# Performance work log

Hardware: AMD Instinct MI355X
Metric: run time of the kernel (lower is better)

The kernel has to match this reference:

```python
import jax, jax.numpy as jnp
import numpy as np

EPS = 1e-6

def _feature_map(x):
    # elu(x) + 1 == where(x>0, x+1, exp(x))
    return jax.nn.elu(x) + 1.0

def setup_inputs() -> dict:
    key = jax.random.key(0)
    kq, kk, kv, km = jax.random.split(key, 4)
    B, H, S, D = 4, 16, 4096, 64
    query = jax.random.normal(kq, (B, H, S, D), dtype=jnp.float32)
    key_t = jax.random.normal(kk, (B, H, S, D), dtype=jnp.float32)
    value = jax.random.normal(kv, (B, H, S, D), dtype=jnp.float32)
    # True = padded position
    key_padding_mask = jax.random.bernoulli(km, 0.25, (B, S))
    return {"query": query, "key": key_t, "value": value,
            "key_padding_mask": key_padding_mask}

def reference(query, key, value, key_padding_mask):
    q = _feature_map(query)              # [B,H,S,D]
    k = _feature_map(key)
    v = value
    # valid = ~mask, broadcast over heads and feature dim
    valid = (~key_padding_mask)[:, None, :, None].astype(query.dtype)  # [B,1,S,1]
    k = k * valid
    v = v * valid
    kv = jnp.einsum('bhsd,bhsf->bhdf', k, v)              # [B,H,D,D]
    z = jnp.einsum('bhtd,bhd->bht', q, k.sum(axis=2)) + EPS
    out = jnp.einsum('bhtd,bhdf->bhtf', q, kv) / z[..., None]
    return out
```

## Files before the change

### kernel.cpp

```cpp
#include <hip/hip_runtime.h>

#define S_LEN 4096
#define D_DIM 64
#define NBH   64
#define EPS_F 1e-6f
#define PSZ   (D_DIM * D_DIM + D_DIM)

__device__ __forceinline__ float phi_f(float x) {
    return x > 0.0f ? x + 1.0f : __expf(x);
}

__global__ void detect_mask(const unsigned int* __restrict__ w,
                            unsigned int* __restrict__ flag) {
    __shared__ int all01, allf;
    if (threadIdx.x == 0) { all01 = 1; allf = 1; }
    __syncthreads();
    int a = 1, f = 1;
    for (int i = threadIdx.x; i < 4096; i += blockDim.x) {
        unsigned int v = w[i];
        if (v > 1u) a = 0;
        if (v != 0u && v != 0x3F800000u) f = 0;
    }
    if (!a) atomicExch(&all01, 0);
    if (!f) atomicExch(&allf, 0);
    __syncthreads();
    if (threadIdx.x == 0) *flag = all01 ? 0u : (allf ? 2u : 1u);
}

__global__ __launch_bounds__(256) void la_phase1(
    const float* __restrict__ K, const float* __restrict__ V,
    const void* __restrict__ mask, const unsigned int* __restrict__ flagp,
    float* __restrict__ partials, int CH)
{
    __shared__ float smem[2][4096];
    __shared__ float ksred[4][64];

    const int bh   = blockIdx.x;
    const int b    = bh >> 4;
    const unsigned int flag = *flagp;
    const int tid  = threadIdx.x;
    const int wave = tid >> 6;
    const int lane = tid & 63;
    const int tt   = lane >> 3;
    const int tf   = lane & 7;
    const int chunk = S_LEN / CH;
    const int NT    = chunk / 32;
    const int s0    = blockIdx.y * chunk;

    const float* Kbh = K + (size_t)bh * S_LEN * D_DIM;
    const float* Vbh = V + (size_t)bh * S_LEN * D_DIM;
    const int*           mi = (const int*)mask;
    const unsigned char* mb = (const unsigned char*)mask;
    const float*         mf = (const float*)mask;

    float acc[8][8];
    float ks[8];
    #pragma unroll
    for (int i = 0; i < 8; ++i) {
        ks[i] = 0.0f;
        #pragma unroll
        for (int j = 0; j < 8; ++j) acc[i][j] = 0.0f;
    }

    const int row0 = tid >> 4;
    const int col0 = (tid & 15) * 4;

    float4 kr[2], vr[2];
    int    pr[2];

    auto issue = [&](int ts) {
        #pragma unroll
        for (int p = 0; p < 2; ++p) {
            int row = p * 16 + row0;
            int s   = s0 + ts + row;
            int ml  = b * S_LEN + s;
            bool pad;
            if (flag == 0u)      pad = (mi[ml] != 0);
            else if (flag == 1u) pad = (mb[ml] != 0);
            else                 pad = (mf[ml] != 0.0f);
            pr[p] = pad ? 1 : 0;
            kr[p] = *reinterpret_cast<const float4*>(&Kbh[(size_t)s * D_DIM + col0]);
            vr[p] = *reinterpret_cast<const float4*>(&Vbh[(size_t)s * D_DIM + col0]);
        }
    };

    auto xstore = [&](int bufi) {
        #pragma unroll
        for (int p = 0; p < 2; ++p) {
            int row = p * 16 + row0;
            float4 k4 = kr[p], v4 = vr[p];
            if (pr[p]) {
                k4 = make_float4(0.f, 0.f, 0.f, 0.f);
                v4 = make_float4(0.f, 0.f, 0.f, 0.f);
            } else {
                k4.x = phi_f(k4.x); k4.y = phi_f(k4.y);
                k4.z = phi_f(k4.z); k4.w = phi_f(k4.w);
            }
            *reinterpret_cast<float4*>(&smem[bufi][row * 64 + col0])        = k4;
            *reinterpret_cast<float4*>(&smem[bufi][2048 + row * 64 + col0]) = v4;
        }
    };

    issue(0);
    xstore(0);
    __syncthreads();
    int cur = 0;
    for (int it = 0; it < NT; ++it) {
        if (it + 1 < NT) issue((it + 1) * 32);
        #pragma unroll
        for (int r = 0; r < 8; ++r) {
            const int row = wave * 8 + r;
            float kk[8], vv[8];
            *reinterpret_cast<float4*>(&kk[0]) = *reinterpret_cast<const float4*>(&smem[cur][row * 64 + tt * 8]);
            *reinterpret_cast<float4*>(&kk[4]) = *reinterpret_cast<const float4*>(&smem[cur][row * 64 + tt * 8 + 4]);
            *reinterpret_cast<float4*>(&vv[0]) = *reinterpret_cast<const float4*>(&smem[cur][2048 + row * 64 + tf * 8]);
            *reinterpret_cast<float4*>(&vv[4]) = *reinterpret_cast<const float4*>(&smem[cur][2048 + row * 64 + tf * 8 + 4]);
            #pragma unroll
            for (int i = 0; i < 8; ++i) {
                #pragma unroll
                for (int j = 0; j < 8; ++j)
                    acc[i][j] = fmaf(kk[i], vv[j], acc[i][j]);
                ks[i] += kk[i];
            }
        }
        if (it + 1 < NT) xstore(cur ^ 1);
        __syncthreads();
        cur ^= 1;
    }

    if (tf == 0) {
        #pragma unroll
        for (int i = 0; i < 8; ++i) ksred[wave][tt * 8 + i] = ks[i];
    }
    for (int w = 0; w < 4; ++w) {
        if (wave == w) {
            #pragma unroll
            for (int i = 0; i < 8; ++i) {
                float4* p0 = reinterpret_cast<float4*>(&smem[0][(tt * 8 + i) * 64 + tf * 8]);
                float4 a0 = make_float4(acc[i][0], acc[i][1], acc[i][2], acc[i][3]);
                float4 a1 = make_float4(acc[i][4], acc[i][5], acc[i][6], acc[i][7]);
                if (w == 0) { p0[0] = a0; p0[1] = a1; }
                else {
                    float4 c0 = p0[0], c1 = p0[1];
                    c0.x += a0.x; c0.y += a0.y; c0.z += a0.z; c0.w += a0.w;
                    c1.x += a1.x; c1.y += a1.y; c1.z += a1.z; c1.w += a1.w;
                    p0[0] = c0; p0[1] = c1;
                }
            }
        }
        __syncthreads();
    }

    float* pp = partials + ((size_t)(bh * CH + blockIdx.y)) * PSZ;
    #pragma unroll
    for (int q = 0; q < 4; ++q) {
        int fi = q * 256 + tid;
        reinterpret_cast<float4*>(pp)[fi] = reinterpret_cast<const float4*>(&smem[0][0])[fi];
    }
    if (tid < 64)
        pp[4096 + tid] = ksred[0][tid] + ksred[1][tid] + ksred[2][tid] + ksred[3][tid];
}

template <int CHT>
__global__ __launch_bounds__(256) void la_reduce_t(
    const float* __restrict__ partials, float* __restrict__ kv,
    float* __restrict__ ksum)
{
    const int bh = blockIdx.x;
    const int half = blockIdx.y;
    const float4* base = reinterpret_cast<const float4*>(partials + (size_t)bh * CHT * PSZ);
    const int hi = (half + 1) * 520;
    for (int idx = half * 520 + threadIdx.x; idx < hi; idx += 256) {
        float4 s = make_float4(0.f, 0.f, 0.f, 0.f);
        #pragma unroll
        for (int c = 0; c < CHT; ++c) {
            float4 v = base[(size_t)c * (PSZ / 4) + idx];
            s.x += v.x; s.y += v.y; s.z += v.z; s.w += v.w;
        }
        if (idx < 1024)
            reinterpret_cast<float4*>(kv + (size_t)bh * 4096)[idx] = s;
        else
            reinterpret_cast<float4*>(ksum + bh * 64)[idx - 1024] = s;
    }
}

__global__ __launch_bounds__(256) void la_phase2(
    const float* __restrict__ Q,
    const float* __restrict__ kv_ws, const float* __restrict__ ksum_ws,
    float* __restrict__ out)
{
    __shared__ float kvs[64][64];
    __shared__ float kss[64];

    const int bh   = blockIdx.x;
    const int tid  = threadIdx.x;
    const int wave = tid >> 6;
    const int lane = tid & 63;
    const int tt   = lane >> 3;
    const int tf   = lane & 7;
    const int t0   = blockIdx.y * 128 + wave * 32;

    const float* Qbh = Q + (size_t)bh * S_LEN * D_DIM;
    const float* kvb = kv_ws + (size_t)bh * D_DIM * D_DIM;

    #pragma unroll
    for (int p = 0; p < 4; ++p) {
        int fi = p * 256 + tid;
        reinterpret_cast<float4*>(kvs)[fi] = reinterpret_cast<const float4*>(kvb)[fi];
    }
    if (tid < 16)
        reinterpret_cast<float4*>(kss)[tid] =
            reinterpret_cast<const float4*>(ksum_ws + bh * D_DIM)[tid];
    __syncthreads();

    const float* qr0 = Qbh + (size_t)(t0 + tt) * D_DIM;

    float acc[4][8];
    float z[4];
    #pragma unroll
    for (int r = 0; r < 4; ++r) {
        z[r] = 0.0f;
        #pragma unroll
        for (int c = 0; c < 8; ++c) acc[r][c] = 0.0f;
    }

    float4 qn[4];
    #pragma unroll
    for (int r = 0; r < 4; ++r)
        qn[r] = *reinterpret_cast<const float4*>(qr0 + r * 8 * D_DIM);

    #pragma unroll 4
    for (int dq = 0; dq < 64; dq += 4) {
        float qc[4][4];
        #pragma unroll
        for (int r = 0; r < 4; ++r) {
            qc[r][0] = phi_f(qn[r].x); qc[r][1] = phi_f(qn[r].y);
            qc[r][2] = phi_f(qn[r].z); qc[r][3] = phi_f(qn[r].w);
        }
        const int dnext = (dq + 4) & 63;
        #pragma unroll
        for (int r = 0; r < 4; ++r)
            qn[r] = *reinterpret_cast<const float4*>(qr0 + r * 8 * D_DIM + dnext);
        float ks4[4];
        *reinterpret_cast<float4*>(ks4) = *reinterpret_cast<const float4*>(&kss[dq]);
        #pragma unroll
        for (int j = 0; j < 4; ++j) {
            float kvr[8];
            *reinterpret_cast<float4*>(&kvr[0]) = *reinterpret_cast<const float4*>(&kvs[dq + j][tf * 8]);
            *reinterpret_cast<float4*>(&kvr[4]) = *reinterpret_cast<const float4*>(&kvs[dq + j][tf * 8 + 4]);
            #pragma unroll
            for (int r = 0; r < 4; ++r) {
                z[r] = fmaf(qc[r][j], ks4[j], z[r]);
                #pragma unroll
                for (int c = 0; c < 8; ++c)
                    acc[r][c] = fmaf(qc[r][j], kvr[c], acc[r][c]);
            }
        }
    }

    #pragma unroll
    for (int r = 0; r < 4; ++r) {
        int t = t0 + tt + 8 * r;
        float inv = 1.0f / (z[r] + EPS_F);
        float o[8];
        #pragma unroll
        for (int c = 0; c < 8; ++c) o[c] = acc[r][c] * inv;
        float* op = out + ((size_t)bh * S_LEN + t) * D_DIM + tf * 8;
        *reinterpret_cast<float4*>(&op[0]) = *reinterpret_cast<const float4*>(&o[0]);
        *reinterpret_cast<float4*>(&op[4]) = *reinterpret_cast<const float4*>(&o[4]);
    }
}

extern "C" void kernel_launch(void* const* d_in, const int* in_sizes, int n_in,
                              void* d_out, int out_size, void* d_ws, size_t ws_size,
                              hipStream_t stream)
{
    (void)in_sizes; (void)n_in; (void)out_size;
    const float* Q   = (const float*)d_in[0];
    const float* K   = (const float*)d_in[1];
    const float* V   = (const float*)d_in[2];
    const void* mask = d_in[3];

    int CH = 16;
    while (CH > 1) {
        size_t need = ((size_t)NBH * CH * PSZ + (size_t)NBH * 4096 + NBH * 64) * 4 + 16;
        if (need <= ws_size) break;
        CH >>= 1;
    }
    float* partials = (float*)d_ws;
    float* kvf  = partials + (size_t)NBH * CH * PSZ;
    float* ksf  = kvf + (size_t)NBH * 4096;
    unsigned int* flag = (unsigned int*)(ksf + NBH * 64);

    detect_mask<<<1, 256, 0, stream>>>((const unsigned int*)mask, flag);
    la_phase1<<<dim3(NBH, CH), 256, 0, stream>>>(K, V, mask, flag, partials, CH);
    switch (CH) {
        case 16: la_reduce_t<16><<<dim3(NBH, 2), 256, 0, stream>>>(partials, kvf, ksf); break;
        case 8:  la_reduce_t<8> <<<dim3(NBH, 2), 256, 0, stream>>>(partials, kvf, ksf); break;
        case 4:  la_reduce_t<4> <<<dim3(NBH, 2), 256, 0, stream>>>(partials, kvf, ksf); break;
        case 2:  la_reduce_t<2> <<<dim3(NBH, 2), 256, 0, stream>>>(partials, kvf, ksf); break;
        default: la_reduce_t<1> <<<dim3(NBH, 2), 256, 0, stream>>>(partials, kvf, ksf); break;
    }
    la_phase2<<<dim3(NBH, 32), 256, 0, stream>>>(Q, kvf, ksf, (float*)d_out);
}
```

Measured before the change: 281.7 us.

## Read K/V and kv state directly from global memory, dropping LDS staging

```diff
diff --git a/kernel.cpp b/kernel.cpp
--- a/kernel.cpp
+++ b/kernel.cpp
@@ -32,7 +32,7 @@
     const void* __restrict__ mask, const unsigned int* __restrict__ flagp,
     float* __restrict__ partials, int CH)
 {
-    __shared__ float smem[2][4096];
+    __shared__ float red[4096];
     __shared__ float ksred[4][64];
 
     const int bh   = blockIdx.x;
@@ -44,14 +44,15 @@
     const int tt   = lane >> 3;
     const int tf   = lane & 7;
     const int chunk = S_LEN / CH;
-    const int NT    = chunk / 32;
-    const int s0    = blockIdx.y * chunk;
-
-    const float* Kbh = K + (size_t)bh * S_LEN * D_DIM;
-    const float* Vbh = V + (size_t)bh * S_LEN * D_DIM;
+    const int rpw   = chunk >> 2;
+    const int s0    = blockIdx.y * chunk + wave * rpw;
+
+    const float* Kr = K + ((size_t)bh * S_LEN + s0) * D_DIM;
+    const float* Vr = V + ((size_t)bh * S_LEN + s0) * D_DIM;
     const int*           mi = (const int*)mask;
     const unsigned char* mb = (const unsigned char*)mask;
     const float*         mf = (const float*)mask;
+    const int ml0 = b * S_LEN + s0;
 
     float acc[8][8];
     float ks[8];
@@ -62,59 +63,27 @@
         for (int j = 0; j < 8; ++j) acc[i][j] = 0.0f;
     }
 
-    const int row0 = tid >> 4;
-    const int col0 = (tid & 15) * 4;
-
-    float4 kr[2], vr[2];
-    int    pr[2];
-
-    auto issue = [&](int ts) {
-        #pragma unroll
-        for (int p = 0; p < 2; ++p) {
-            int row = p * 16 + row0;
-            int s   = s0 + ts + row;
-            int ml  = b * S_LEN + s;
-            bool pad;
-            if (flag == 0u)      pad = (mi[ml] != 0);
-            else if (flag == 1u) pad = (mb[ml] != 0);
-            else                 pad = (mf[ml] != 0.0f);
-            pr[p] = pad ? 1 : 0;
-            kr[p] = *reinterpret_cast<const float4*>(&Kbh[(size_t)s * D_DIM + col0]);
-            vr[p] = *reinterpret_cast<const float4*>(&Vbh[(size_t)s * D_DIM + col0]);
-        }
-    };
-
-    auto xstore = [&](int bufi) {
-        #pragma unroll
-        for (int p = 0; p < 2; ++p) {
-            int row = p * 16 + row0;
-            float4 k4 = kr[p], v4 = vr[p];
-            if (pr[p]) {
-                k4 = make_float4(0.f, 0.f, 0.f, 0.f);
-                v4 = make_float4(0.f, 0.f, 0.f, 0.f);
-            } else {
-                k4.x = phi_f(k4.x); k4.y = phi_f(k4.y);
-                k4.z = phi_f(k4.z); k4.w = phi_f(k4.w);
-            }
-            *reinterpret_cast<float4*>(&smem[bufi][row * 64 + col0])        = k4;
-            *reinterpret_cast<float4*>(&smem[bufi][2048 + row * 64 + col0]) = v4;
-        }
-    };
-
-    issue(0);
-    xstore(0);
-    __syncthreads();
-    int cur = 0;
-    for (int it = 0; it < NT; ++it) {
-        if (it + 1 < NT) issue((it + 1) * 32);
-        #pragma unroll
-        for (int r = 0; r < 8; ++r) {
-            const int row = wave * 8 + r;
+    for (int seg = 0; seg < rpw; seg += 64) {
+        int mvi;
+        {
+            const int ml = ml0 + seg + lane;
+            if (flag == 0u)      mvi = (mi[ml] != 0);
+            else if (flag == 1u) mvi = (mb[ml] != 0);
+            else                 mvi = (mf[ml] != 0.0f);
+        }
+        const float* Ks = Kr + (size_t)seg * D_DIM;
+        const float* Vs = Vr + (size_t)seg * D_DIM;
+        #pragma unroll 2
+        for (int r = 0; r < 64; ++r) {
+            const int pad = __shfl(mvi, r);
             float kk[8], vv[8];
-            *reinterpret_cast<float4*>(&kk[0]) = *reinterpret_cast<const float4*>(&smem[cur][row * 64 + tt * 8]);
-            *reinterpret_cast<float4*>(&kk[4]) = *reinterpret_cast<const float4*>(&smem[cur][row * 64 + tt * 8 + 4]);
-            *reinterpret_cast<float4*>(&vv[0]) = *reinterpret_cast<const float4*>(&smem[cur][2048 + row * 64 + tf * 8]);
-            *reinterpret_cast<float4*>(&vv[4]) = *reinterpret_cast<const float4*>(&smem[cur][2048 + row * 64 + tf * 8 + 4]);
+            *reinterpret_cast<float4*>(&kk[0]) = *reinterpret_cast<const float4*>(Ks + r * 64 + tt * 8);
+            *reinterpret_cast<float4*>(&kk[4]) = *reinterpret_cast<const float4*>(Ks + r * 64 + tt * 8 + 4);
+            *reinterpret_cast<float4*>(&vv[0]) = *reinterpret_cast<const float4*>(Vs + r * 64 + tf * 8);
+            *reinterpret_cast<float4*>(&vv[4]) = *reinterpret_cast<const float4*>(Vs + r * 64 + tf * 8 + 4);
+            #pragma unroll
+            for (int i = 0; i < 8; ++i)
+                kk[i] = pad ? 0.0f : phi_f(kk[i]);
             #pragma unroll
             for (int i = 0; i < 8; ++i) {
                 #pragma unroll
@@ -123,20 +92,18 @@
                 ks[i] += kk[i];
             }
         }
-        if (it + 1 < NT) xstore(cur ^ 1);
-        __syncthreads();
-        cur ^= 1;
     }
 
     if (tf == 0) {
         #pragma unroll
         for (int i = 0; i < 8; ++i) ksred[wave][tt * 8 + i] = ks[i];
     }
+    __syncthreads();
     for (int w = 0; w < 4; ++w) {
         if (wave == w) {
             #pragma unroll
             for (int i = 0; i < 8; ++i) {
-                float4* p0 = reinterpret_cast<float4*>(&smem[0][(tt * 8 + i) * 64 + tf * 8]);
+                float4* p0 = reinterpret_cast<float4*>(&red[(tt * 8 + i) * 64 + tf * 8]);
                 float4 a0 = make_float4(acc[i][0], acc[i][1], acc[i][2], acc[i][3]);
                 float4 a1 = make_float4(acc[i][4], acc[i][5], acc[i][6], acc[i][7]);
                 if (w == 0) { p0[0] = a0; p0[1] = a1; }
@@ -155,7 +122,7 @@
     #pragma unroll
     for (int q = 0; q < 4; ++q) {
         int fi = q * 256 + tid;
-        reinterpret_cast<float4*>(pp)[fi] = reinterpret_cast<const float4*>(&smem[0][0])[fi];
+        reinterpret_cast<float4*>(pp)[fi] = reinterpret_cast<const float4*>(red)[fi];
     }
     if (tid < 64)
         pp[4096 + tid] = ksred[0][tid] + ksred[1][tid] + ksred[2][tid] + ksred[3][tid];
@@ -189,9 +156,6 @@
     const float* __restrict__ kv_ws, const float* __restrict__ ksum_ws,
     float* __restrict__ out)
 {
-    __shared__ float kvs[64][64];
-    __shared__ float kss[64];
-
     const int bh   = blockIdx.x;
     const int tid  = threadIdx.x;
     const int wave = tid >> 6;
@@ -200,20 +164,9 @@
     const int tf   = lane & 7;
     const int t0   = blockIdx.y * 128 + wave * 32;
 
-    const float* Qbh = Q + (size_t)bh * S_LEN * D_DIM;
+    const float* qr0 = Q + ((size_t)bh * S_LEN + t0 + tt) * D_DIM;
     const float* kvb = kv_ws + (size_t)bh * D_DIM * D_DIM;
-
-    #pragma unroll
-    for (int p = 0; p < 4; ++p) {
-        int fi = p * 256 + tid;
-        reinterpret_cast<float4*>(kvs)[fi] = reinterpret_cast<const float4*>(kvb)[fi];
-    }
-    if (tid < 16)
-        reinterpret_cast<float4*>(kss)[tid] =
-            reinterpret_cast<const float4*>(ksum_ws + bh * D_DIM)[tid];
-    __syncthreads();
-
-    const float* qr0 = Qbh + (size_t)(t0 + tt) * D_DIM;
+    const float* ksb = ksum_ws + bh * D_DIM;
 
     float acc[4][8];
     float z[4];
@@ -224,30 +177,22 @@
         for (int c = 0; c < 8; ++c) acc[r][c] = 0.0f;
     }
 
-    float4 qn[4];
-    #pragma unroll
-    for (int r = 0; r < 4; ++r)
-        qn[r] = *reinterpret_cast<const float4*>(qr0 + r * 8 * D_DIM);
-
-    #pragma unroll 4
+    #pragma unroll 2
     for (int dq = 0; dq < 64; dq += 4) {
+        float ks4[4];
+        *reinterpret_cast<float4*>(ks4) = *reinterpret_cast<const float4*>(ksb + dq);
         float qc[4][4];
         #pragma unroll
         for (int r = 0; r < 4; ++r) {
-            qc[r][0] = phi_f(qn[r].x); qc[r][1] = phi_f(qn[r].y);
-            qc[r][2] = phi_f(qn[r].z); qc[r][3] = phi_f(qn[r].w);
-        }
-        const int dnext = (dq + 4) & 63;
-        #pragma unroll
-        for (int r = 0; r < 4; ++r)
-            qn[r] = *reinterpret_cast<const float4*>(qr0 + r * 8 * D_DIM + dnext);
-        float ks4[4];
-        *reinterpret_cast<float4*>(ks4) = *reinterpret_cast<const float4*>(&kss[dq]);
+            float4 q4 = *reinterpret_cast<const float4*>(qr0 + r * 8 * D_DIM + dq);
+            qc[r][0] = phi_f(q4.x); qc[r][1] = phi_f(q4.y);
+            qc[r][2] = phi_f(q4.z); qc[r][3] = phi_f(q4.w);
+        }
         #pragma unroll
         for (int j = 0; j < 4; ++j) {
             float kvr[8];
-            *reinterpret_cast<float4*>(&kvr[0]) = *reinterpret_cast<const float4*>(&kvs[dq + j][tf * 8]);
-            *reinterpret_cast<float4*>(&kvr[4]) = *reinterpret_cast<const float4*>(&kvs[dq + j][tf * 8 + 4]);
+            *reinterpret_cast<float4*>(&kvr[0]) = *reinterpret_cast<const float4*>(kvb + (dq + j) * 64 + tf * 8);
+            *reinterpret_cast<float4*>(&kvr[4]) = *reinterpret_cast<const float4*>(kvb + (dq + j) * 64 + tf * 8 + 4);
             #pragma unroll
             for (int r = 0; r < 4; ++r) {
                 z[r] = fmaf(qc[r][j], ks4[j], z[r]);
```

Result: slower. 352.6 us (+25.2%).

## Double phase1 threads, split D across waves, stage mask in LDS

Applied to the files above, without the earlier changes.

```diff
diff --git a/kernel.cpp b/kernel.cpp
--- a/kernel.cpp
+++ b/kernel.cpp
@@ -27,22 +27,25 @@
     if (threadIdx.x == 0) *flag = all01 ? 0u : (allf ? 2u : 1u);
 }
 
-__global__ __launch_bounds__(256) void la_phase1(
+__global__ __launch_bounds__(512) void la_phase1(
     const float* __restrict__ K, const float* __restrict__ V,
     const void* __restrict__ mask, const unsigned int* __restrict__ flagp,
     float* __restrict__ partials, int CH)
 {
     __shared__ float smem[2][4096];
+    __shared__ float mlds[2][32];
     __shared__ float ksred[4][64];
 
     const int bh   = blockIdx.x;
     const int b    = bh >> 4;
     const unsigned int flag = *flagp;
     const int tid  = threadIdx.x;
-    const int wave = tid >> 6;
+    const int wv   = tid >> 6;
     const int lane = tid & 63;
-    const int tt   = lane >> 3;
-    const int tf   = lane & 7;
+    const int rq   = wv >> 1;
+    const int dh   = wv & 1;
+    const int dgrp = lane >> 3;
+    const int fgrp = lane & 7;
     const int chunk = S_LEN / CH;
     const int NT    = chunk / 32;
     const int s0    = blockIdx.y * chunk;
@@ -53,52 +56,42 @@
     const unsigned char* mb = (const unsigned char*)mask;
     const float*         mf = (const float*)mask;
 
-    float acc[8][8];
-    float ks[8];
-    #pragma unroll
-    for (int i = 0; i < 8; ++i) {
+    float acc[4][8];
+    float ks[4];
+    #pragma unroll
+    for (int i = 0; i < 4; ++i) {
         ks[i] = 0.0f;
         #pragma unroll
         for (int j = 0; j < 8; ++j) acc[i][j] = 0.0f;
     }
 
-    const int row0 = tid >> 4;
-    const int col0 = (tid & 15) * 4;
-
-    float4 kr[2], vr[2];
-    int    pr[2];
+    const int srow = tid >> 4;
+    const int scol = (tid & 15) * 4;
+
+    float4 kr, vr;
+    float  mreg = 1.0f;
 
     auto issue = [&](int ts) {
-        #pragma unroll
-        for (int p = 0; p < 2; ++p) {
-            int row = p * 16 + row0;
-            int s   = s0 + ts + row;
-            int ml  = b * S_LEN + s;
+        const int s = s0 + ts + srow;
+        kr = *reinterpret_cast<const float4*>(&Kbh[(size_t)s * D_DIM + scol]);
+        vr = *reinterpret_cast<const float4*>(&Vbh[(size_t)s * D_DIM + scol]);
+        if (tid < 32) {
+            const int ml = b * S_LEN + s0 + ts + tid;
             bool pad;
             if (flag == 0u)      pad = (mi[ml] != 0);
             else if (flag == 1u) pad = (mb[ml] != 0);
             else                 pad = (mf[ml] != 0.0f);
-            pr[p] = pad ? 1 : 0;
-            kr[p] = *reinterpret_cast<const float4*>(&Kbh[(size_t)s * D_DIM + col0]);
-            vr[p] = *reinterpret_cast<const float4*>(&Vbh[(size_t)s * D_DIM + col0]);
+            mreg = pad ? 0.0f : 1.0f;
         }
     };
 
     auto xstore = [&](int bufi) {
-        #pragma unroll
-        for (int p = 0; p < 2; ++p) {
-            int row = p * 16 + row0;
-            float4 k4 = kr[p], v4 = vr[p];
-            if (pr[p]) {
-                k4 = make_float4(0.f, 0.f, 0.f, 0.f);
-                v4 = make_float4(0.f, 0.f, 0.f, 0.f);
-            } else {
-                k4.x = phi_f(k4.x); k4.y = phi_f(k4.y);
-                k4.z = phi_f(k4.z); k4.w = phi_f(k4.w);
-            }
-            *reinterpret_cast<float4*>(&smem[bufi][row * 64 + col0])        = k4;
-            *reinterpret_cast<float4*>(&smem[bufi][2048 + row * 64 + col0]) = v4;
-        }
+        float4 k4 = kr;
+        k4.x = phi_f(k4.x); k4.y = phi_f(k4.y);
+        k4.z = phi_f(k4.z); k4.w = phi_f(k4.w);
+        *reinterpret_cast<float4*>(&smem[bufi][srow * 64 + scol])        = k4;
+        *reinterpret_cast<float4*>(&smem[bufi][2048 + srow * 64 + scol]) = vr;
+        if (tid < 32) mlds[bufi][tid] = mreg;
     };
 
     issue(0);
@@ -107,16 +100,20 @@
     int cur = 0;
     for (int it = 0; it < NT; ++it) {
         if (it + 1 < NT) issue((it + 1) * 32);
+        const float* kb = &smem[cur][(rq * 8) * 64 + dh * 32 + dgrp * 4];
+        const float* vb = &smem[cur][2048 + (rq * 8) * 64 + fgrp * 8];
+        const float* mp = &mlds[cur][rq * 8];
         #pragma unroll
         for (int r = 0; r < 8; ++r) {
-            const int row = wave * 8 + r;
-            float kk[8], vv[8];
-            *reinterpret_cast<float4*>(&kk[0]) = *reinterpret_cast<const float4*>(&smem[cur][row * 64 + tt * 8]);
-            *reinterpret_cast<float4*>(&kk[4]) = *reinterpret_cast<const float4*>(&smem[cur][row * 64 + tt * 8 + 4]);
-            *reinterpret_cast<float4*>(&vv[0]) = *reinterpret_cast<const float4*>(&smem[cur][2048 + row * 64 + tf * 8]);
-            *reinterpret_cast<float4*>(&vv[4]) = *reinterpret_cast<const float4*>(&smem[cur][2048 + row * 64 + tf * 8 + 4]);
+            const float m = mp[r];
+            float kk[4], vv[8];
+            *reinterpret_cast<float4*>(&kk[0]) = *reinterpret_cast<const float4*>(kb + r * 64);
+            *reinterpret_cast<float4*>(&vv[0]) = *reinterpret_cast<const float4*>(vb + r * 64);
+            *reinterpret_cast<float4*>(&vv[4]) = *reinterpret_cast<const float4*>(vb + r * 64 + 4);
             #pragma unroll
-            for (int i = 0; i < 8; ++i) {
+            for (int i = 0; i < 4; ++i) kk[i] *= m;
+            #pragma unroll
+            for (int i = 0; i < 4; ++i) {
                 #pragma unroll
                 for (int j = 0; j < 8; ++j)
                     acc[i][j] = fmaf(kk[i], vv[j], acc[i][j]);
@@ -128,18 +125,23 @@
         cur ^= 1;
     }
 
-    if (tf == 0) {
-        #pragma unroll
-        for (int i = 0; i < 8; ++i) ksred[wave][tt * 8 + i] = ks[i];
-    }
-    for (int w = 0; w < 4; ++w) {
-        if (wave == w) {
+    if (fgrp == 0) {
+        #pragma unroll
+        for (int i = 0; i < 4; ++i)
+            ksred[rq][dh * 32 + dgrp * 4 + i] = ks[i];
+    }
+    __syncthreads();
+
+    float* red = smem[0];
+    for (int q = 0; q < 4; ++q) {
+        if (rq == q) {
             #pragma unroll
-            for (int i = 0; i < 8; ++i) {
-                float4* p0 = reinterpret_cast<float4*>(&smem[0][(tt * 8 + i) * 64 + tf * 8]);
+            for (int i = 0; i < 4; ++i) {
+                float4* p0 = reinterpret_cast<float4*>(
+                    &red[(dh * 32 + dgrp * 4 + i) * 64 + fgrp * 8]);
                 float4 a0 = make_float4(acc[i][0], acc[i][1], acc[i][2], acc[i][3]);
                 float4 a1 = make_float4(acc[i][4], acc[i][5], acc[i][6], acc[i][7]);
-                if (w == 0) { p0[0] = a0; p0[1] = a1; }
+                if (q == 0) { p0[0] = a0; p0[1] = a1; }
                 else {
                     float4 c0 = p0[0], c1 = p0[1];
                     c0.x += a0.x; c0.y += a0.y; c0.z += a0.z; c0.w += a0.w;
@@ -153,9 +155,9 @@
 
     float* pp = partials + ((size_t)(bh * CH + blockIdx.y)) * PSZ;
     #pragma unroll
-    for (int q = 0; q < 4; ++q) {
-        int fi = q * 256 + tid;
-        reinterpret_cast<float4*>(pp)[fi] = reinterpret_cast<const float4*>(&smem[0][0])[fi];
+    for (int q = 0; q < 2; ++q) {
+        int fi = q * 512 + tid;
+        reinterpret_cast<float4*>(pp)[fi] = reinterpret_cast<const float4*>(red)[fi];
     }
     if (tid < 64)
         pp[4096 + tid] = ksred[0][tid] + ksred[1][tid] + ksred[2][tid] + ksred[3][tid];
@@ -224,23 +226,26 @@
         for (int c = 0; c < 8; ++c) acc[r][c] = 0.0f;
     }
 
-    float4 qn[4];
-    #pragma unroll
-    for (int r = 0; r < 4; ++r)
-        qn[r] = *reinterpret_cast<const float4*>(qr0 + r * 8 * D_DIM);
-
-    #pragma unroll 4
+    float4 qn0[4], qn1[4];
+    #pragma unroll
+    for (int r = 0; r < 4; ++r) {
+        qn0[r] = *reinterpret_cast<const float4*>(qr0 + r * 8 * D_DIM);
+        qn1[r] = *reinterpret_cast<const float4*>(qr0 + r * 8 * D_DIM + 4);
+    }
+
+    #pragma unroll
     for (int dq = 0; dq < 64; dq += 4) {
         float qc[4][4];
         #pragma unroll
         for (int r = 0; r < 4; ++r) {
-            qc[r][0] = phi_f(qn[r].x); qc[r][1] = phi_f(qn[r].y);
-            qc[r][2] = phi_f(qn[r].z); qc[r][3] = phi_f(qn[r].w);
-        }
-        const int dnext = (dq + 4) & 63;
+            qc[r][0] = phi_f(qn0[r].x); qc[r][1] = phi_f(qn0[r].y);
+            qc[r][2] = phi_f(qn0[r].z); qc[r][3] = phi_f(qn0[r].w);
+            qn0[r] = qn1[r];
+        }
+        const int dnext = (dq + 8) & 63;
         #pragma unroll
         for (int r = 0; r < 4; ++r)
-            qn[r] = *reinterpret_cast<const float4*>(qr0 + r * 8 * D_DIM + dnext);
+            qn1[r] = *reinterpret_cast<const float4*>(qr0 + r * 8 * D_DIM + dnext);
         float ks4[4];
         *reinterpret_cast<float4*>(ks4) = *reinterpret_cast<const float4*>(&kss[dq]);
         #pragma unroll
@@ -293,7 +298,7 @@
     unsigned int* flag = (unsigned int*)(ksf + NBH * 64);
 
     detect_mask<<<1, 256, 0, stream>>>((const unsigned int*)mask, flag);
-    la_phase1<<<dim3(NBH, CH), 256, 0, stream>>>(K, V, mask, flag, partials, CH);
+    la_phase1<<<dim3(NBH, CH), 512, 0, stream>>>(K, V, mask, flag, partials, CH);
     switch (CH) {
         case 16: la_reduce_t<16><<<dim3(NBH, 2), 256, 0, stream>>>(partials, kvf, ksf); break;
         case 8:  la_reduce_t<8> <<<dim3(NBH, 2), 256, 0, stream>>>(partials, kvf, ksf); break;
```

New measurement: 291.9 us. +3.6%, slower.
